# Performance work log

Measured on AMD Instinct MI355X. Metric: run time of the kernel, lower is better.

## Reference

```python
import jax, jax.numpy as jnp
import numpy as np

K = 9
STRIDE = 1
UNFOLDINGS = 12
N_SIGMA = 1
SIGMA_MIN, SIGMA_MAX = 0.0, 50.0


def soft_threshold(x, lmbda):
    return jnp.sign(x) * jnp.maximum(jnp.abs(x) - lmbda, 0.0)


def lookup_arr(value):
    # arr = [sigma_min + d*i for i in range(n_sigma+1)], d=(max-min)/n_sigma
    d = (SIGMA_MAX - SIGMA_MIN) / N_SIGMA
    arr = [SIGMA_MIN + d * i for i in range(N_SIGMA + 1)]
    for i, x in enumerate(arr):
        if value <= x:
            return max(i - 1, 0)
    return len(arr) - 2


def im2col(I, k, s):
    # torch F.unfold ordering: channel-major, then kh, kw -> [B, C*k*k, Ho, Wo]
    B, C, H, W = I.shape
    Ho = (H - k) // s + 1
    Wo = (W - k) // s + 1
    cols = jnp.stack(
        [I[:, :, i:i + (Ho - 1) * s + 1:s, j:j + (Wo - 1) * s + 1:s]
         for i in range(k) for j in range(k)], axis=2)  # [B, C, k*k, Ho, Wo]
    return cols.reshape(B, C * k * k, Ho, Wo)


def col2im_avg(cols, H, W, k, s):
    # F.fold with averaging by overlap counts
    B, Ckk, Ho, Wo = cols.shape
    C = Ckk // (k * k)
    x = cols.reshape(B, C, k, k, Ho, Wo)
    out = jnp.zeros((B, C, H, W), cols.dtype)
    cnt = jnp.zeros((1, 1, H, W), cols.dtype)
    one = jnp.ones((1, 1, Ho, Wo), cols.dtype)
    for i in range(k):
        for j in range(k):
            sl_h = slice(i, i + (Ho - 1) * s + 1, s)
            sl_w = slice(j, j + (Wo - 1) * s + 1, s)
            out = out.at[:, :, sl_h, sl_w].add(x[:, :, i, j])
            cnt = cnt.at[:, :, sl_h, sl_w].add(one)
    return out / cnt


def setup_inputs() -> dict:
    key = jax.random.key(0)
    k1, k2 = jax.random.split(key)
    Ckk = K * K * 3  # 243
    F = 256
    I = jax.random.normal(k1, (4, 3, 128, 128), dtype=jnp.float32)
    # Dictionary init normalized by sqrt of top singular value ~ spectral norm
    D = jax.random.normal(k2, (Ckk, F), dtype=jnp.float32)
    s_max = jnp.linalg.norm(D.T @ D, ord=2)
    D = D / jnp.sqrt(s_max)
    A = D.T                      # [F, Ckk]
    Dw = jnp.array(D)            # [Ckk, F]
    Ww = jnp.array(D)            # [Ckk, F]
    lmbdas = jnp.full((UNFOLDINGS, F), 0.01, dtype=jnp.float32)
    return {"I": I, "A": A, "Dw": Dw, "Ww": Ww, "lmbdas": lmbdas, "sigma_hat": 25}


def reference(I, A, Dw, Ww, lmbdas, sigma_hat):
    noise_set = lookup_arr(sigma_hat)  # python int, trace-time constant
    B, C, H, W = I.shape
    I_col = im2col(I, K, STRIDE)                     # [B, Ckk, Ho, Wo]
    mean_patch = I_col.mean(axis=1, keepdims=True)   # centered patches
    I_c = I_col - mean_patch
    lin = jnp.einsum('fc,bchw->bfhw', A, I_c)
    lm = lmbdas[noise_set * UNFOLDINGS][None, :, None, None]
    gamma = soft_threshold(lin, lm)
    for kk in range(UNFOLDINGS - 1):
        x_k = jnp.einsum('cf,bfhw->bchw', Dw, gamma)
        r_k = jnp.einsum('fc,bchw->bfhw', A, x_k - I_c)
        lm = lmbdas[noise_set * UNFOLDINGS + kk + 1][None, :, None, None]
        gamma = soft_threshold(gamma - r_k, lm)
    out_all = jnp.einsum('cf,bfhw->bchw', Ww, gamma) + mean_patch
    return col2im_avg(out_all, H, W, K, STRIDE)
```

## Files before the change

kernel.cpp:

```cpp
#include <hip/hip_runtime.h>
#include <stdint.h>

typedef __attribute__((ext_vector_type(8))) short bf16x8;
typedef __attribute__((ext_vector_type(4))) float f32x4;

__device__ __forceinline__ unsigned short f2bf(float f) {
  union { float f; unsigned u; } v; v.f = f;
  unsigned u = v.u;
  u += 0x7fffu + ((u >> 16) & 1u);
  return (unsigned short)(u >> 16);
}

__device__ __forceinline__ int swz_idx(int k, int n) {
  return ((((k >> 5) * 16 + (n >> 4)) * 64) + (((k >> 3) & 3) * 16 + (n & 15))) * 8 + (k & 7);
}

#define LM_STRIDE 264

__device__ float g_rowmean[256];
__device__ __attribute__((aligned(16))) unsigned short g_Acswz[65536];
__device__ __attribute__((aligned(16))) unsigned short g_Gswz[65536];
__device__ __attribute__((aligned(16))) unsigned short g_W3swz[65536];


__global__ void prep_rowmean(const float* __restrict__ A) {
  int f = threadIdx.x;
  float s = 0.f;
  for (int c = 0; c < 243; ++c) s += A[f * 243 + c];
  g_rowmean[f] = s * (1.f / 243.f);
}

__global__ void prep_Ac(const float* __restrict__ A) {
  int k = blockIdx.x;
  int n = threadIdx.x;
  float v = 0.f;
  if (k < 243) {
    int rw = k / 9, j = k - rw * 9;
    int i = rw / 3, c = rw - i * 3;
    int corig = c * 81 + i * 9 + j;
    v = A[n * 243 + corig] - g_rowmean[n];
  }
  g_Acswz[swz_idx(k, n)] = f2bf(v);
}

__global__ void prep_G(const float* __restrict__ A, const float* __restrict__ Dw) {
  int f = blockIdx.x;
  int fp = threadIdx.x;
  float s = 0.f;
  for (int c = 0; c < 243; ++c) s += A[f * 243 + c] * Dw[c * 256 + fp];
  float v = ((f == fp) ? 1.f : 0.f) - s;
  g_Gswz[swz_idx(fp, f)] = f2bf(v);
}

__global__ void prep_W3(const float* __restrict__ Ww) {
  int cc = blockIdx.x;
  int f = threadIdx.x;
  float v = 0.f;
  if (cc < 243) {
    int rw = cc / 9, j = cc - rw * 9;
    int i = rw / 3, c = rw - i * 3;
    int corig = c * 81 + i * 9 + j;
    v = Ww[corig * 256 + f];
  }
  g_W3swz[swz_idx(f, cc)] = f2bf(v);
}

__global__ void zero_out(float* __restrict__ out, int n) {
  int idx = blockIdx.x * 256 + threadIdx.x;
  if (idx < n) out[idx] = 0.f;
}


__global__ __launch_bounds__(256, 2) void lista_fused(
    const float* __restrict__ I, const float* __restrict__ lmb, float* __restrict__ out) {
  __shared__ float img[3][16][16];
  __shared__ __attribute__((aligned(16))) unsigned short stage[64 * LM_STRIDE];
  __shared__ float meanv[64];
  __shared__ float outacc[768];
  __shared__ float lmbs[12 * 256];

  const int tid = threadIdx.x;
  const int lane = tid & 63;
  const int w = tid >> 6;
  const int m = lane & 15;
  const int q = lane >> 4;

  const int blk = blockIdx.x;
  const int b = blk / 225;
  const int t2 = blk - b * 225;
  const int ty = t2 / 15;
  const int tx = t2 - ty * 15;
  const int py0 = ty * 8, px0 = tx * 8;

  const float* Ib = I + b * (3 * 128 * 128);
  for (int r = tid; r < 768; r += 256) {
    int c = r >> 8;
    int yx = r & 255;
    int y = yx >> 4, x = yx & 15;
    img[c][y][x] = Ib[c * 16384 + (py0 + y) * 128 + (px0 + x)];
    outacc[r] = 0.f;
  }
  for (int r = tid; r < 12 * 256; r += 256) lmbs[r] = lmb[r];
  if (tid < 64) meanv[tid] = 0.f;
  __syncthreads();

  {
    const int p = tid & 63;
    const int part = tid >> 6;
    const int y = p >> 3, x = p & 7;
    int k0 = part * 61;
    int k1 = k0 + 61;
    if (k1 > 243) k1 = 243;
    int rw = k0 / 9;
    int jj = k0 - rw * 9;
    int i = rw / 3, c = rw - i * 3;
    float s = 0.f;
    for (int k = k0; k < k1; ++k) {
      s += img[c][y + i][x + jj];
      if (++jj == 9) { jj = 0; if (++c == 3) { c = 0; ++i; } }
    }
    atomicAdd(&meanv[p], s * (1.f / 243.f));
  }

  f32x4 acc[4][4];
  f32x4 lin[4][4];
  const f32x4 zero = {0.f, 0.f, 0.f, 0.f};

  #pragma unroll
  for (int t = 0; t < 4; ++t)
    #pragma unroll
    for (int un = 0; un < 4; ++un) acc[t][un] = zero;

  #pragma unroll
  for (int s = 0; s < 8; ++s) {
    bf16x8 bf[4];
    #pragma unroll
    for (int un = 0; un < 4; ++un) {
      int u = 4 * w + un;
      bf[un] = *(const bf16x8*)(g_Acswz + (((s * 16 + u) * 64 + lane) << 3));
    }
    #pragma unroll
    for (int t = 0; t < 4; ++t) {
      int p = t * 16 + m;
      int y = p >> 3, x = p & 7;
      int k0 = s * 32 + q * 8;
      int rw = k0 / 9;
      int jj = k0 - rw * 9;
      int i = rw / 3, c = rw - i * 3;
      bf16x8 a;
      #pragma unroll
      for (int j = 0; j < 8; ++j) {
        int k = k0 + j;
        float v = 0.f;
        if (k < 243) v = img[c][y + i][x + jj];
        a[j] = (short)f2bf(v);
        if (++jj == 9) { jj = 0; if (++c == 3) { c = 0; ++i; } }
      }
      #pragma unroll
      for (int un = 0; un < 4; ++un)
        acc[t][un] = __builtin_amdgcn_mfma_f32_16x16x32_bf16(a, bf[un], acc[t][un], 0, 0, 0);
    }
  }

  #pragma unroll
  for (int un = 0; un < 4; ++un) {
    int f = 64 * w + un * 16 + m;
    float lam = lmbs[f];
    #pragma unroll
    for (int t = 0; t < 4; ++t) {
      lin[t][un] = acc[t][un];
      #pragma unroll
      for (int r = 0; r < 4; ++r) {
        float x0 = acc[t][un][r];
        float g = copysignf(fmaxf(fabsf(x0) - lam, 0.f), x0);
        stage[(t * 16 + q * 4 + r) * LM_STRIDE + f] = f2bf(g);
      }
    }
  }
  __syncthreads();

  for (int kk = 0; kk < 11; ++kk) {
    #pragma unroll
    for (int t = 0; t < 4; ++t)
      #pragma unroll
      for (int un = 0; un < 4; ++un) acc[t][un] = lin[t][un];

    #pragma unroll
    for (int s = 0; s < 8; ++s) {
      bf16x8 bf[4];
      #pragma unroll
      for (int un = 0; un < 4; ++un) {
        int u = 4 * w + un;
        bf[un] = *(const bf16x8*)(g_Gswz + (((s * 16 + u) * 64 + lane) << 3));
      }
      #pragma unroll
      for (int t = 0; t < 4; ++t) {
        bf16x8 a = *(const bf16x8*)(&stage[(t * 16 + m) * LM_STRIDE + s * 32 + q * 8]);
        #pragma unroll
        for (int un = 0; un < 4; ++un)
          acc[t][un] = __builtin_amdgcn_mfma_f32_16x16x32_bf16(a, bf[un], acc[t][un], 0, 0, 0);
      }
    }
    __syncthreads();
    #pragma unroll
    for (int un = 0; un < 4; ++un) {
      int f = 64 * w + un * 16 + m;
      float lam = lmbs[(kk + 1) * 256 + f];
      #pragma unroll
      for (int t = 0; t < 4; ++t)
        #pragma unroll
        for (int r = 0; r < 4; ++r) {
          float x0 = acc[t][un][r];
          float g = copysignf(fmaxf(fabsf(x0) - lam, 0.f), x0);
          stage[(t * 16 + q * 4 + r) * LM_STRIDE + f] = f2bf(g);
        }
    }
    __syncthreads();
  }

  #pragma unroll
  for (int t = 0; t < 4; ++t)
    #pragma unroll
    for (int un = 0; un < 4; ++un) acc[t][un] = zero;

  #pragma unroll
  for (int s = 0; s < 8; ++s) {
    bf16x8 bf[4];
    #pragma unroll
    for (int un = 0; un < 4; ++un) {
      int u = 4 * w + un;
      bf[un] = *(const bf16x8*)(g_W3swz + (((s * 16 + u) * 64 + lane) << 3));
    }
    #pragma unroll
    for (int t = 0; t < 4; ++t) {
      bf16x8 a = *(const bf16x8*)(&stage[(t * 16 + m) * LM_STRIDE + s * 32 + q * 8]);
      #pragma unroll
      for (int un = 0; un < 4; ++un)
        acc[t][un] = __builtin_amdgcn_mfma_f32_16x16x32_bf16(a, bf[un], acc[t][un], 0, 0, 0);
    }
  }

  #pragma unroll
  for (int un = 0; un < 4; ++un) {
    int cc = 64 * w + un * 16 + m;
    if (cc < 243) {
      int rw = cc / 9, jj = cc - rw * 9;
      int i = rw / 3, c = rw - i * 3;
      #pragma unroll
      for (int t = 0; t < 4; ++t)
        #pragma unroll
        for (int r = 0; r < 4; ++r) {
          int pos = t * 16 + q * 4 + r;
          int y = (pos >> 3) + i, x = (pos & 7) + jj;
          float val = acc[t][un][r] + meanv[pos];
          atomicAdd(&outacc[c * 256 + y * 16 + x], val);
        }
    }
  }
  __syncthreads();

  float* Ob = out + b * (3 * 128 * 128);
  for (int r = tid; r < 768; r += 256) {
    int c = r >> 8;
    int yx = r & 255;
    int y = yx >> 4, x = yx & 15;
    atomicAdd(&Ob[c * 16384 + (py0 + y) * 128 + (px0 + x)], outacc[r]);
  }
}

__global__ void div_counts(float* __restrict__ out, int n) {
  int idx = blockIdx.x * 256 + threadIdx.x;
  if (idx >= n) return;
  int x = idx & 127, y = (idx >> 7) & 127;
  int loy = y - 8; if (loy < 0) loy = 0;
  int hiy = y; if (hiy > 119) hiy = 119;
  int lox = x - 8; if (lox < 0) lox = 0;
  int hix = x; if (hix > 119) hix = 119;
  float cnt = (float)((hiy - loy + 1) * (hix - lox + 1));
  out[idx] = out[idx] / cnt;
}

extern "C" void kernel_launch(void* const* d_in, const int* in_sizes, int n_in,
                              void* d_out, int out_size, void* d_ws, size_t ws_size,
                              hipStream_t stream) {
  const float* I = (const float*)d_in[0];
  const float* A = (const float*)d_in[1];
  const float* Dw = (const float*)d_in[2];
  const float* Ww = (const float*)d_in[3];
  const float* lmb = (const float*)d_in[4];
  float* out = (float*)d_out;
  (void)d_ws; (void)ws_size;

  const int nblk = (out_size + 255) / 256;
  zero_out<<<nblk, 256, 0, stream>>>(out, out_size);
  prep_rowmean<<<1, 256, 0, stream>>>(A);
  prep_Ac<<<256, 256, 0, stream>>>(A);
  prep_G<<<256, 256, 0, stream>>>(A, Dw);
  prep_W3<<<256, 256, 0, stream>>>(Ww);
  lista_fused<<<900, 256, 0, stream>>>(I, lmb, out);
  div_counts<<<nblk, 256, 0, stream>>>(out, out_size);
}
```

Before: 303.5 us.

## Merge prep kernels, stage im2col in LDS, pack lin in bf16, raise occupancy

Folds the zero, rowmean and three weight-prep kernels into one launch. Builds the im2col tile in shared memory once, so the first GEMM reuses the shared run_gemm path instead of gathering inside the MFMA loop. Stores the lin accumulator as packed bf16 to free registers, raising launch bounds from 2 to 3 waves/SIMD, and prefetches B fragments one step ahead. It also uses a cheaper soft-threshold formula and a padded stage stride. Packing lin to bf16 loses precision in the residual term, and the new div_counts grid size is hardcoded.

Result: slower. 498.6 us (+64.3%).

```diff
diff --git a/kernel.cpp b/kernel.cpp
--- a/kernel.cpp
+++ b/kernel.cpp
@@ -2,6 +2,7 @@
 #include <stdint.h>
 
 typedef __attribute__((ext_vector_type(8))) short bf16x8;
+typedef __attribute__((ext_vector_type(4))) short bf16x4;
 typedef __attribute__((ext_vector_type(4))) float f32x4;
 
 __device__ __forceinline__ unsigned short f2bf(float f) {
@@ -10,71 +11,122 @@
   u += 0x7fffu + ((u >> 16) & 1u);
   return (unsigned short)(u >> 16);
 }
+__device__ __forceinline__ float bfpk_lo(unsigned pk) {
+  union { unsigned u; float f; } v; v.u = pk << 16; return v.f;
+}
+__device__ __forceinline__ float bfpk_hi(unsigned pk) {
+  union { unsigned u; float f; } v; v.u = pk & 0xffff0000u; return v.f;
+}
 
 __device__ __forceinline__ int swz_idx(int k, int n) {
   return ((((k >> 5) * 16 + (n >> 4)) * 64) + (((k >> 3) & 3) * 16 + (n & 15))) * 8 + (k & 7);
 }
 
-#define LM_STRIDE 264
-
-__device__ float g_rowmean[256];
+#define ST_STRIDE 268
+
 __device__ __attribute__((aligned(16))) unsigned short g_Acswz[65536];
 __device__ __attribute__((aligned(16))) unsigned short g_Gswz[65536];
 __device__ __attribute__((aligned(16))) unsigned short g_W3swz[65536];
 
-
-__global__ void prep_rowmean(const float* __restrict__ A) {
-  int f = threadIdx.x;
-  float s = 0.f;
-  for (int c = 0; c < 243; ++c) s += A[f * 243 + c];
-  g_rowmean[f] = s * (1.f / 243.f);
-}
-
-__global__ void prep_Ac(const float* __restrict__ A) {
-  int k = blockIdx.x;
-  int n = threadIdx.x;
-  float v = 0.f;
-  if (k < 243) {
-    int rw = k / 9, j = k - rw * 9;
-    int i = rw / 3, c = rw - i * 3;
-    int corig = c * 81 + i * 9 + j;
-    v = A[n * 243 + corig] - g_rowmean[n];
-  }
-  g_Acswz[swz_idx(k, n)] = f2bf(v);
-}
-
-__global__ void prep_G(const float* __restrict__ A, const float* __restrict__ Dw) {
-  int f = blockIdx.x;
-  int fp = threadIdx.x;
-  float s = 0.f;
-  for (int c = 0; c < 243; ++c) s += A[f * 243 + c] * Dw[c * 256 + fp];
-  float v = ((f == fp) ? 1.f : 0.f) - s;
-  g_Gswz[swz_idx(fp, f)] = f2bf(v);
-}
-
-__global__ void prep_W3(const float* __restrict__ Ww) {
-  int cc = blockIdx.x;
-  int f = threadIdx.x;
-  float v = 0.f;
-  if (cc < 243) {
-    int rw = cc / 9, j = cc - rw * 9;
-    int i = rw / 3, c = rw - i * 3;
-    int corig = c * 81 + i * 9 + j;
-    v = Ww[corig * 256 + f];
-  }
-  g_W3swz[swz_idx(f, cc)] = f2bf(v);
-}
-
-__global__ void zero_out(float* __restrict__ out, int n) {
-  int idx = blockIdx.x * 256 + threadIdx.x;
-  if (idx < n) out[idx] = 0.f;
-}
-
-
-__global__ __launch_bounds__(256, 2) void lista_fused(
+__global__ void prep_all(const float* __restrict__ A, const float* __restrict__ Dw,
+                         const float* __restrict__ Ww, float* __restrict__ out) {
+  __shared__ float red[256];
+  const int b = blockIdx.x;
+  const int tid = threadIdx.x;
+  out[b * 256 + tid] = 0.f;
+
+  if (b < 256) {
+    float s = 0.f;
+    for (int c = tid; c < 243; c += 256) s += A[b * 243 + c];
+    red[tid] = s;
+    __syncthreads();
+    for (int off = 128; off; off >>= 1) {
+      if (tid < off) red[tid] += red[tid + off];
+      __syncthreads();
+    }
+    float rm = red[0] * (1.f / 243.f);
+    int k = tid;
+    float v = 0.f;
+    if (k < 243) {
+      int rw = k / 9, j = k - rw * 9;
+      int i = rw / 3, c = rw - i * 3;
+      int corig = c * 81 + i * 9 + j;
+      v = A[b * 243 + corig] - rm;
+    }
+    g_Acswz[swz_idx(k, b)] = f2bf(v);
+  } else if (b < 512) {
+    int f = b - 256, fp = tid;
+    float s = 0.f;
+    for (int c = 0; c < 243; ++c) s += A[f * 243 + c] * Dw[c * 256 + fp];
+    g_Gswz[swz_idx(fp, f)] = f2bf(((f == fp) ? 1.f : 0.f) - s);
+  } else {
+    int cc = b - 512, f = tid;
+    float v = 0.f;
+    if (cc < 243) {
+      int rw = cc / 9, j = cc - rw * 9;
+      int i = rw / 3, c = rw - i * 3;
+      int corig = c * 81 + i * 9 + j;
+      v = Ww[corig * 256 + f];
+    }
+    g_W3swz[swz_idx(f, cc)] = f2bf(v);
+  }
+}
+
+template <int CMODE>
+__device__ __forceinline__ void run_gemm(const unsigned short* __restrict__ Bsrc,
+                                         const unsigned short* stg, int w, int lane,
+                                         int m, int q, f32x4 (&acc)[4][4],
+                                         unsigned (*linpk)[4][2]) {
+  bf16x8 bcur[4];
+#pragma unroll
+  for (int un = 0; un < 4; ++un)
+    bcur[un] = *(const bf16x8*)(Bsrc + (((4 * w + un) * 64 + lane) << 3));
+#pragma unroll
+  for (int s = 0; s < 8; ++s) {
+    bf16x8 bnext[4];
+    if (s < 7) {
+#pragma unroll
+      for (int un = 0; un < 4; ++un)
+        bnext[un] = *(const bf16x8*)(Bsrc + ((((s + 1) * 16 + 4 * w + un) * 64 + lane) << 3));
+    }
+    bf16x8 afr[4];
+#pragma unroll
+    for (int t = 0; t < 4; ++t) {
+      const unsigned short* ap = stg + (t * 16 + m) * ST_STRIDE + s * 32 + q * 8;
+      bf16x4 lo = *(const bf16x4*)(ap);
+      bf16x4 hi = *(const bf16x4*)(ap + 4);
+      afr[t] = __builtin_shufflevector(lo, hi, 0, 1, 2, 3, 4, 5, 6, 7);
+    }
+#pragma unroll
+    for (int t = 0; t < 4; ++t)
+#pragma unroll
+      for (int un = 0; un < 4; ++un) {
+        f32x4 cin;
+        if (s == 0) {
+          if (CMODE == 1) {
+            cin[0] = bfpk_lo(linpk[t][un][0]);
+            cin[1] = bfpk_hi(linpk[t][un][0]);
+            cin[2] = bfpk_lo(linpk[t][un][1]);
+            cin[3] = bfpk_hi(linpk[t][un][1]);
+          } else {
+            cin = (f32x4){0.f, 0.f, 0.f, 0.f};
+          }
+        } else {
+          cin = acc[t][un];
+        }
+        acc[t][un] = __builtin_amdgcn_mfma_f32_16x16x32_bf16(afr[t], bcur[un], cin, 0, 0, 0);
+      }
+    if (s < 7) {
+#pragma unroll
+      for (int un = 0; un < 4; ++un) bcur[un] = bnext[un];
+    }
+  }
+}
+
+__global__ __launch_bounds__(256, 3) void lista_fused(
     const float* __restrict__ I, const float* __restrict__ lmb, float* __restrict__ out) {
   __shared__ float img[3][16][16];
-  __shared__ __attribute__((aligned(16))) unsigned short stage[64 * LM_STRIDE];
+  __shared__ __attribute__((aligned(16))) unsigned short stage[64 * ST_STRIDE];
   __shared__ float meanv[64];
   __shared__ float outacc[768];
   __shared__ float lmbs[12 * 256];
@@ -105,150 +157,78 @@
   __syncthreads();
 
   {
-    const int p = tid & 63;
+    const int pos = tid & 63;
     const int part = tid >> 6;
-    const int y = p >> 3, x = p & 7;
-    int k0 = part * 61;
-    int k1 = k0 + 61;
-    if (k1 > 243) k1 = 243;
-    int rw = k0 / 9;
-    int jj = k0 - rw * 9;
-    int i = rw / 3, c = rw - i * 3;
+    const int y = pos >> 3, x = pos & 7;
+    int j = part, c = 0, i = 0;
     float s = 0.f;
-    for (int k = k0; k < k1; ++k) {
-      s += img[c][y + i][x + jj];
-      if (++jj == 9) { jj = 0; if (++c == 3) { c = 0; ++i; } }
-    }
-    atomicAdd(&meanv[p], s * (1.f / 243.f));
-  }
+    unsigned short* srow = &stage[pos * ST_STRIDE];
+    for (int kk = 0; kk < 64; ++kk) {
+      int k = part + 4 * kk;
+      float v = 0.f;
+      if (k < 243) { v = img[c][y + i][x + j]; s += v; }
+      srow[k] = f2bf(v);
+      j += 4;
+      if (j >= 9) { j -= 9; if (++c == 3) { c = 0; ++i; } }
+    }
+    atomicAdd(&meanv[pos], s * (1.f / 243.f));
+  }
+  __syncthreads();
 
   f32x4 acc[4][4];
-  f32x4 lin[4][4];
-  const f32x4 zero = {0.f, 0.f, 0.f, 0.f};
-
-  #pragma unroll
-  for (int t = 0; t < 4; ++t)
-    #pragma unroll
-    for (int un = 0; un < 4; ++un) acc[t][un] = zero;
-
-  #pragma unroll
-  for (int s = 0; s < 8; ++s) {
-    bf16x8 bf[4];
-    #pragma unroll
-    for (int un = 0; un < 4; ++un) {
-      int u = 4 * w + un;
-      bf[un] = *(const bf16x8*)(g_Acswz + (((s * 16 + u) * 64 + lane) << 3));
-    }
-    #pragma unroll
-    for (int t = 0; t < 4; ++t) {
-      int p = t * 16 + m;
-      int y = p >> 3, x = p & 7;
-      int k0 = s * 32 + q * 8;
-      int rw = k0 / 9;
-      int jj = k0 - rw * 9;
-      int i = rw / 3, c = rw - i * 3;
-      bf16x8 a;
-      #pragma unroll
-      for (int j = 0; j < 8; ++j) {
-        int k = k0 + j;
-        float v = 0.f;
-        if (k < 243) v = img[c][y + i][x + jj];
-        a[j] = (short)f2bf(v);
-        if (++jj == 9) { jj = 0; if (++c == 3) { c = 0; ++i; } }
-      }
-      #pragma unroll
-      for (int un = 0; un < 4; ++un)
-        acc[t][un] = __builtin_amdgcn_mfma_f32_16x16x32_bf16(a, bf[un], acc[t][un], 0, 0, 0);
-    }
-  }
-
-  #pragma unroll
+  unsigned linpk[4][4][2];
+
+  run_gemm<0>(g_Acswz, stage, w, lane, m, q, acc, linpk);
+  __syncthreads();
+
+#pragma unroll
   for (int un = 0; un < 4; ++un) {
     int f = 64 * w + un * 16 + m;
     float lam = lmbs[f];
-    #pragma unroll
+#pragma unroll
     for (int t = 0; t < 4; ++t) {
-      lin[t][un] = acc[t][un];
-      #pragma unroll
+      linpk[t][un][0] = (unsigned)f2bf(acc[t][un][0]) | ((unsigned)f2bf(acc[t][un][1]) << 16);
+      linpk[t][un][1] = (unsigned)f2bf(acc[t][un][2]) | ((unsigned)f2bf(acc[t][un][3]) << 16);
+#pragma unroll
       for (int r = 0; r < 4; ++r) {
         float x0 = acc[t][un][r];
-        float g = copysignf(fmaxf(fabsf(x0) - lam, 0.f), x0);
-        stage[(t * 16 + q * 4 + r) * LM_STRIDE + f] = f2bf(g);
+        float g = x0 - fminf(fmaxf(x0, -lam), lam);
+        stage[(t * 16 + q * 4 + r) * ST_STRIDE + f] = f2bf(g);
       }
     }
   }
   __syncthreads();
 
   for (int kk = 0; kk < 11; ++kk) {
-    #pragma unroll
-    for (int t = 0; t < 4; ++t)
-      #pragma unroll
-      for (int un = 0; un < 4; ++un) acc[t][un] = lin[t][un];
-
-    #pragma unroll
-    for (int s = 0; s < 8; ++s) {
-      bf16x8 bf[4];
-      #pragma unroll
-      for (int un = 0; un < 4; ++un) {
-        int u = 4 * w + un;
-        bf[un] = *(const bf16x8*)(g_Gswz + (((s * 16 + u) * 64 + lane) << 3));
-      }
-      #pragma unroll
-      for (int t = 0; t < 4; ++t) {
-        bf16x8 a = *(const bf16x8*)(&stage[(t * 16 + m) * LM_STRIDE + s * 32 + q * 8]);
-        #pragma unroll
-        for (int un = 0; un < 4; ++un)
-          acc[t][un] = __builtin_amdgcn_mfma_f32_16x16x32_bf16(a, bf[un], acc[t][un], 0, 0, 0);
-      }
-    }
+    run_gemm<1>(g_Gswz, stage, w, lane, m, q, acc, linpk);
     __syncthreads();
-    #pragma unroll
+#pragma unroll
     for (int un = 0; un < 4; ++un) {
       int f = 64 * w + un * 16 + m;
       float lam = lmbs[(kk + 1) * 256 + f];
-      #pragma unroll
+#pragma unroll
       for (int t = 0; t < 4; ++t)
-        #pragma unroll
+#pragma unroll
         for (int r = 0; r < 4; ++r) {
           float x0 = acc[t][un][r];
-          float g = copysignf(fmaxf(fabsf(x0) - lam, 0.f), x0);
-          stage[(t * 16 + q * 4 + r) * LM_STRIDE + f] = f2bf(g);
+          float g = x0 - fminf(fmaxf(x0, -lam), lam);
+          stage[(t * 16 + q * 4 + r) * ST_STRIDE + f] = f2bf(g);
         }
     }
     __syncthreads();
   }
 
-  #pragma unroll
-  for (int t = 0; t < 4; ++t)
-    #pragma unroll
-    for (int un = 0; un < 4; ++un) acc[t][un] = zero;
-
-  #pragma unroll
-  for (int s = 0; s < 8; ++s) {
-    bf16x8 bf[4];
-    #pragma unroll
-    for (int un = 0; un < 4; ++un) {
-      int u = 4 * w + un;
-      bf[un] = *(const bf16x8*)(g_W3swz + (((s * 16 + u) * 64 + lane) << 3));
-    }
-    #pragma unroll
-    for (int t = 0; t < 4; ++t) {
-      bf16x8 a = *(const bf16x8*)(&stage[(t * 16 + m) * LM_STRIDE + s * 32 + q * 8]);
-      #pragma unroll
-      for (int un = 0; un < 4; ++un)
-        acc[t][un] = __builtin_amdgcn_mfma_f32_16x16x32_bf16(a, bf[un], acc[t][un], 0, 0, 0);
-    }
-  }
-
-  #pragma unroll
+  run_gemm<0>(g_W3swz, stage, w, lane, m, q, acc, linpk);
+
+#pragma unroll
   for (int un = 0; un < 4; ++un) {
     int cc = 64 * w + un * 16 + m;
     if (cc < 243) {
       int rw = cc / 9, jj = cc - rw * 9;
       int i = rw / 3, c = rw - i * 3;
-      #pragma unroll
+#pragma unroll
       for (int t = 0; t < 4; ++t)
-        #pragma unroll
+#pragma unroll
         for (int r = 0; r < 4; ++r) {
           int pos = t * 16 + q * 4 + r;
           int y = (pos >> 3) + i, x = (pos & 7) + jj;
@@ -291,12 +271,7 @@
   float* out = (float*)d_out;
   (void)d_ws; (void)ws_size;
 
-  const int nblk = (out_size + 255) / 256;
-  zero_out<<<nblk, 256, 0, stream>>>(out, out_size);
-  prep_rowmean<<<1, 256, 0, stream>>>(A);
-  prep_Ac<<<256, 256, 0, stream>>>(A);
-  prep_G<<<256, 256, 0, stream>>>(A, Dw);
-  prep_W3<<<256, 256, 0, stream>>>(Ww);
+  prep_all<<<768, 256, 0, stream>>>(A, Dw, Ww, out);
   lista_fused<<<900, 256, 0, stream>>>(I, lmb, out);
-  div_counts<<<nblk, 256, 0, stream>>>(out, out_size);
-}
+  div_counts<<<768, 256, 0, stream>>>(out, out_size);
+}
```
